# Performance work log

Measured on AMD Instinct MI355X. Metric: run time of the kernel, lower is better.

The kernel has to match this reference:

```python
import jax, jax.numpy as jnp
import numpy as np

V, E, H, D = 50257, 512, 512, 2  # vocab, embed_dim, hidden_dim, depth (nlayers)
B, S, T = 32, 60, 48             # batch, encoder len, target len


def setup_inputs() -> dict:
    key = jax.random.key(0)
    ks = jax.random.split(key, 9)
    return {
        "enc_h": jax.random.normal(ks[0], (B, S, 2 * H), jnp.float32),
        "prev_s": jax.random.normal(ks[1], (B, H), jnp.float32),
        "target": jax.random.randint(ks[2], (T, B), 0, V),
        "embed_W": jax.random.normal(ks[3], (V, E), jnp.float32) * 0.02,
        "attn_W": jax.random.normal(ks[4], (2 * H, H), jnp.float32) * (1.0 / np.sqrt(2 * H)),
        "attn_b": jnp.zeros((H,), jnp.float32),
        "inp_W": jax.random.normal(ks[5], (E, 2 * H), jnp.float32) * (1.0 / np.sqrt(E)),
        "inp_b": jnp.zeros((2 * H,), jnp.float32),
        "cell_W": jax.random.normal(ks[6], (D, H, 2 * H), jnp.float32) * (1.0 / np.sqrt(H)),
        "cell_b": jnp.zeros((D, 2 * H), jnp.float32),
        "out_W": jax.random.normal(ks[7], (H, V), jnp.float32) * (1.0 / np.sqrt(H)),
        "out_b": jnp.zeros((V,), jnp.float32),
    }


def reference(enc_h, prev_s, target, embed_W, attn_W, attn_b,
              inp_W, inp_b, cell_W, cell_b, out_W, out_b):
    # target: T x B -> embeddings T x B x E
    emb = embed_W[target]
    # enc_h is fixed across timesteps: precompute attention keys (B x S x H)
    energy = jnp.tanh(enc_h @ attn_W + attn_b)
    depth = cell_W.shape[0]

    def step(s, x_t):
        # attention: scores B x S, ctx B x 2H
        scores = jnp.einsum("bsh,bh->bs", energy, s)
        alpha = jax.nn.softmax(scores, axis=-1)
        ctx = jnp.einsum("bs,bsd->bd", alpha, enc_h)
        ctx_e = ctx[:, :E]  # module uses ctx[:, 0:embed_dim] (j never updated)
        for l in range(depth):  # small fixed depth loop
            Ws = (s * ctx_e) @ cell_W[l] + cell_b[l]
            if l == 0:
                Ws = Ws + x_t @ inp_W + inp_b
            hh, tt = jnp.split(Ws, 2, axis=1)
            hh = jnp.tanh(hh)
            tt = jax.nn.sigmoid(tt)
            s = hh * tt + s * (1.0 - tt)  # highway gate (dropout p=0)
        return s, s

    _, dec_h = jax.lax.scan(step, prev_s, emb)  # T x B x H
    return dec_h @ out_W + out_b  # T x B x V
```

## Files before the change

kernel.cpp:

```cpp
#include <hip/hip_runtime.h>
#include <hip/hip_bf16.h>
#include <math.h>

#define B_ 32
#define S_ 60
#define T_ 48
#define H_ 512
#define E_ 512
#define V_ 50257
#define NPAD 50432
#define EPI_LD 260
#define NTILE ((NPAD / 256) * 12)

typedef __attribute__((ext_vector_type(8))) short bf16x8v;
typedef __attribute__((ext_vector_type(4))) float f32x4v;
typedef __attribute__((ext_vector_type(4))) float f32x4a __attribute__((aligned(4)));
typedef __attribute__((ext_vector_type(4))) unsigned int u32x4;

__device__ inline unsigned short f2bf(float f) {
    union { float f; unsigned u; } v; v.f = f;
    unsigned r = v.u + 0x7fffu + ((v.u >> 16) & 1u);
    return (unsigned short)(r >> 16);
}
__device__ inline float bflo(unsigned u) { return __uint_as_float(u << 16); }

__device__ inline void gload_lds16(const void* g, void* l) {
    __builtin_amdgcn_global_load_lds(
        (const __attribute__((address_space(1))) unsigned int*)g,
        (__attribute__((address_space(3))) unsigned int*)l, 16, 0, 0);
}

__device__ __forceinline__ float ld_coh_f32_nw(const float* p) {
    float r;
    asm volatile("global_load_dword %0, %1, off sc0 sc1"
                 : "=v"(r) : "v"(p) : "memory");
    return r;
}
__device__ __forceinline__ void st_coh_f32(float* p, float v) {
    asm volatile("global_store_dword %0, %1, off sc0 sc1"
                 :: "v"(p), "v"(v) : "memory");
}
__device__ __forceinline__ void st_coh_u16(unsigned short* p, unsigned int v) {
    asm volatile("global_store_short %0, %1, off sc0 sc1"
                 :: "v"(p), "v"(v) : "memory");
}
__device__ __forceinline__ void st_coh_u32(int* p, int v) {
    asm volatile("global_store_dword %0, %1, off sc0 sc1"
                 :: "v"(p), "v"(v) : "memory");
}
__device__ __forceinline__ void st_coh_u64(unsigned long long* p, unsigned long long v) {
    asm volatile("global_store_dwordx2 %0, %1, off sc0 sc1"
                 :: "v"(p), "v"(v) : "memory");
}
__device__ __forceinline__ int ld_coh_u32(const int* p) {
    int r;
    asm volatile("global_load_dword %0, %1, off sc0 sc1\n\ts_waitcnt vmcnt(0)"
                 : "=v"(r) : "v"(p) : "memory");
    return r;
}
__device__ __forceinline__ u32x4 ld_cohx4(const void* p) {
    u32x4 r;
    asm volatile("global_load_dwordx4 %0, %1, off sc0 sc1"
                 : "=v"(r) : "v"(p) : "memory");
    return r;
}

__device__ __forceinline__ void gbar(int* flags, int idx, int bi) {
    asm volatile("s_waitcnt vmcnt(0)" ::: "memory");
    __syncthreads();
    if (threadIdx.x == 0)
        st_coh_u32(&flags[idx * 32 + bi], 1);
    if (threadIdx.x < 64) {
        const int* fp = &flags[idx * 32 + (threadIdx.x & 31)];
        for (;;) {
            int v = ld_coh_u32(fp);
            if (__all(v != 0)) break;
            __builtin_amdgcn_s_sleep(1);
        }
    }
    __syncthreads();
}

template<int ACT, bool GATHER>
__device__ void gemm_body(const float* __restrict__ A, const float* __restrict__ Bm,
                          const float* __restrict__ bias, float* __restrict__ C,
                          int N, int K, int lda, const int* __restrict__ gidx,
                          int cb, int rb, float (*As)[128], float (*Bs)[128])
{
    const int tid = threadIdx.x;
    const int am = tid >> 1;
    const int ak = (tid & 1) * 4;
    const int arow = rb + am;
    const float* Arow;
    if (GATHER) Arow = A + (size_t)gidx[arow] * lda;
    else        Arow = A + (size_t)arow * lda;

    const int bk = tid >> 5;
    const int bn = (tid & 31) * 4;

    const int tx = tid & 15, ty = tid >> 4;
    float acc[8][8];
    #pragma unroll
    for (int i = 0; i < 8; i++)
        #pragma unroll
        for (int j = 0; j < 8; j++) acc[i][j] = 0.f;

    for (int k0 = 0; k0 < K; k0 += 8) {
        float4 av = *(const float4*)(Arow + k0 + ak);
        float4 bv = *(const float4*)(Bm + (size_t)(k0 + bk) * N + cb + bn);
        __syncthreads();
        As[ak + 0][am] = av.x; As[ak + 1][am] = av.y;
        As[ak + 2][am] = av.z; As[ak + 3][am] = av.w;
        Bs[bk][bn + 0] = bv.x; Bs[bk][bn + 1] = bv.y;
        Bs[bk][bn + 2] = bv.z; Bs[bk][bn + 3] = bv.w;
        __syncthreads();

        #pragma unroll
        for (int k = 0; k < 8; k++) {
            float a[8], b[8];
            *(float4*)(a)     = *(const float4*)&As[k][ty * 4];
            *(float4*)(a + 4) = *(const float4*)&As[k][ty * 4 + 64];
            *(float4*)(b)     = *(const float4*)&Bs[k][tx * 4];
            *(float4*)(b + 4) = *(const float4*)&Bs[k][tx * 4 + 64];
            #pragma unroll
            for (int i = 0; i < 8; i++)
                #pragma unroll
                for (int j = 0; j < 8; j++)
                    acc[i][j] = fmaf(a[i], b[j], acc[i][j]);
        }
    }

    #pragma unroll
    for (int i = 0; i < 8; i++) {
        int row = rb + ((i < 4) ? (ty * 4 + i) : (64 + ty * 4 + (i - 4)));
        #pragma unroll
        for (int j = 0; j < 8; j++) {
            int col = cb + ((j < 4) ? (tx * 4 + j) : (64 + tx * 4 + (j - 4)));
            float v = acc[i][j] + bias[col];
            if (ACT == 1) v = tanhf(v);
            C[(size_t)row * N + col] = v;
        }
    }
}

__global__ __launch_bounds__(256)
void gemm_pro(const float* __restrict__ enc_h, const float* __restrict__ attn_W,
              const float* __restrict__ attn_b, float* __restrict__ energy,
              const float* __restrict__ embed_W, const float* __restrict__ inp_W,
              const float* __restrict__ inp_b, float* __restrict__ pre,
              const int* __restrict__ target, int* __restrict__ cnt)
{
    __shared__ float As[8][128];
    __shared__ float Bs[8][128];
    const int bx = blockIdx.x;
    if (bx < 60) {
        const int cb = (bx & 3) * 128, rb = (bx >> 2) * 128;
        gemm_body<1, false>(enc_h, attn_W, attn_b, energy,
                            512, 1024, 1024, nullptr, cb, rb, As, Bs);
    } else if (bx < 156) {
        const int b2 = bx - 60;
        const int cb = (b2 & 7) * 128, rb = (b2 >> 3) * 128;
        gemm_body<0, true>(embed_W, inp_W, inp_b, pre,
                           1024, 512, 512, target, cb, rb, As, Bs);
    } else {
        for (int i = threadIdx.x; i < 144 * 32; i += 256)
            st_coh_u32(&cnt[i], 0);
    }
}

union __align__(16) ScanSM {
    struct {
        float eL[S_][H_];
        float part[8 * 32 * 36];
        float sCol[512];
    } s;
    float til[2 * 32 * 33];
    char g[49152];
};

template<int LI>
__device__ __forceinline__ void highway(
    int t, int bi, int tid, int lane, int wv,
    const bf16x8v (&wf)[2][2],
    const unsigned short* __restrict__ xsrc,
    unsigned short* __restrict__ xG1,
    const float* __restrict__ ctxG,
    float* __restrict__ sG,
    unsigned short* __restrict__ dec_b,
    const float* __restrict__ pre,
    float cbh, float cbt,
    float* part, float* sCol)
{
    const int l15 = lane & 15, lc = lane >> 4;
    const int b = tid >> 4, hi = tid & 15;
    const int h = bi * 16 + hi;

    float cxv = 0.f, prh = 0.f, prt = 0.f;
    if (LI == 0) {
        cxv = ld_coh_f32_nw(ctxG + (size_t)b * 512 + h);
        const float* pr = pre + ((size_t)t * B_ + b) * 1024;
        prh = pr[h]; prt = pr[h + 512];
    }

    u32x4 xr[2][2][2];
    #pragma unroll
    for (int ktl = 0; ktl < 2; ++ktl)
        #pragma unroll
        for (int pl = 0; pl < 2; ++pl)
            #pragma unroll
            for (int mt = 0; mt < 2; ++mt) {
                int ch = (((wv * 2 + ktl) * 2 + pl) * 4 + lc) * 32 + mt * 16 + l15;
                xr[ktl][pl][mt] = ld_cohx4(xsrc + (size_t)ch * 8);
            }
    asm volatile("s_waitcnt vmcnt(0)" ::: "memory");
    __builtin_amdgcn_sched_barrier(0);

    f32x4v acc[2][2];
    #pragma unroll
    for (int mt = 0; mt < 2; ++mt)
        #pragma unroll
        for (int nt = 0; nt < 2; ++nt) acc[mt][nt] = (f32x4v)0.f;

    #pragma unroll
    for (int ktl = 0; ktl < 2; ++ktl)
        #pragma unroll
        for (int pl = 0; pl < 2; ++pl)
            #pragma unroll
            for (int mt = 0; mt < 2; ++mt) {
                bf16x8v xv = *(bf16x8v*)&xr[ktl][pl][mt];
                #pragma unroll
                for (int nt = 0; nt < 2; ++nt)
                    acc[mt][nt] = __builtin_amdgcn_mfma_f32_16x16x32_bf16(
                        wf[ktl][nt], xv, acc[mt][nt], 0, 0, 0);
            }

    #pragma unroll
    for (int mt = 0; mt < 2; ++mt)
        #pragma unroll
        for (int nt = 0; nt < 2; ++nt)
            *(f32x4v*)&part[(wv * 32 + mt * 16 + l15) * 36 + nt * 16 + lc * 4] = acc[mt][nt];
    __syncthreads();

    float rh = 0.f, rt = 0.f;
    #pragma unroll
    for (int w = 0; w < 8; ++w) {
        rh += part[(w * 32 + b) * 36 + hi];
        rt += part[(w * 32 + b) * 36 + 16 + hi];
    }
    float ph = rh + cbh, pt = rt + cbt;
    if (LI == 0) { ph += prh; pt += prt; }
    float hh = tanhf(ph);
    float tg = 1.f / (1.f + __expf(-pt));
    float sold = sCol[tid];
    float sn = hh * tg + sold * (1.f - tg);
    sCol[tid] = sn;
    if (LI == 0) {
        float x1 = sn * cxv;
        unsigned short xh = f2bf(x1);
        unsigned short xl = f2bf(x1 - bflo((unsigned)xh));
        int kt = h >> 5, lc2 = (h >> 3) & 3, jj = h & 7;
        int ch = (kt * 8 + lc2) * 32 + b;
        st_coh_u16(xG1 + (size_t)ch * 8 + jj, xh);
        st_coh_u16(xG1 + (size_t)(ch + 128) * 8 + jj, xl);
    } else {
        st_coh_f32(sG + ((size_t)bi * 32 + b) * 16 + hi, sn);
        st_coh_u16(dec_b + ((size_t)bi * 1536 + (size_t)t * B_ + b) * 16 + hi,
                   f2bf(sn));
    }
}

__global__ __launch_bounds__(512, 2)
void scan_tr(const float* __restrict__ energy, const float* __restrict__ enc_h,
             const float* __restrict__ prev_s, const float* __restrict__ pre,
             const float* __restrict__ cell_W, const float* __restrict__ cell_b,
             unsigned short* __restrict__ dec_b,
             const float* __restrict__ outW, unsigned short* __restrict__ Wt,
             float* __restrict__ ctxG, float* __restrict__ sG,
             unsigned short* __restrict__ xG0, unsigned short* __restrict__ xG1,
             int* __restrict__ cnt,
             const float* __restrict__ out_b, float* __restrict__ out)
{
    __shared__ ScanSM sm;
    const int tid = threadIdx.x;

    if (blockIdx.x >= B_) {
        const int hb = blockIdx.x - B_;
        const int g = tid >> 8;
        const int tt0 = tid & 255;
        const int r = tt0 >> 3, c4 = (tt0 & 7) * 4;
        float* til = sm.til;
        #pragma unroll 1
        for (int j = 0; j < 57; ++j) {
            const int tt = hb * 2 + g + j * 448;
            const bool act = tt < (NPAD / 32) * 16;
            int n0 = 0, k0 = 0;
            if (act) {
                n0 = (tt >> 4) * 32;
                k0 = (tt & 15) * 32;
                #pragma unroll
                for (int jj = 0; jj < 4; ++jj) {
                    int n = n0 + c4 + jj;
                    til[(g * 32 + r) * 33 + c4 + jj] =
                        (n < V_) ? __builtin_nontemporal_load(&outW[(size_t)(k0 + r) * V_ + n]) : 0.f;
                }
            }
            __syncthreads();
            if (act) {
                const int n = n0 + r;
                unsigned lo = (unsigned)f2bf(til[(g * 32 + c4 + 0) * 33 + r])
                            | ((unsigned)f2bf(til[(g * 32 + c4 + 1) * 33 + r]) << 16);
                unsigned hi2 = (unsigned)f2bf(til[(g * 32 + c4 + 2) * 33 + r])
                             | ((unsigned)f2bf(til[(g * 32 + c4 + 3) * 33 + r]) << 16);
                unsigned long long ov = (unsigned long long)lo | ((unsigned long long)hi2 << 32);
                st_coh_u64((unsigned long long*)&Wt[(size_t)n * 512 + k0 + c4], ov);
            }
            __syncthreads();
        }

        {
            int* hF = cnt + 101 * 32;
            asm volatile("s_waitcnt vmcnt(0)" ::: "memory");
            __syncthreads();
            if (tid == 0) st_coh_u32(&hF[hb], 1);
            if (tid < 64) {
                for (;;) {
                    int ok = 1;
                    #pragma unroll
                    for (int q = 0; q < 4; ++q) {
                        int idx = (tid & 63) + q * 64;
                        int v = (idx < 224) ? ld_coh_u32(&hF[idx]) : 1;
                        ok &= (v != 0);
                    }
                    if (__all(ok)) break;
                    __builtin_amdgcn_s_sleep(16);
                }
            }
            __syncthreads();
        }

        {
            short* As_wt  = (short*)sm.g;
            short* Bs_dec = (short*)(sm.g + 32768);
            float* epi    = (float*)sm.g;
            const int lane = tid & 63, w = tid >> 6;
            const int wm = w >> 2, wn = w & 3;
            int* sF = cnt + 100 * 32;

#define STAGE_TILE(bix, kt, rb, cb) do {                                      \
            short* Ab_ = As_wt + (bix) * 8192;                                \
            short* Bb_ = Bs_dec + (bix) * 4096;                               \
            _Pragma("unroll")                                                 \
            for (int j_ = 0; j_ < 2; ++j_) {                                  \
                int rg_ = w * 2 + j_;                                         \
                int row_ = rg_ * 16 + (lane >> 2);                            \
                int kc_ = (lane & 3) ^ (row_ & 3);                            \
                gload_lds16(Wt + ((size_t)((cb) + row_) * 512 + (kt) * 32 + kc_ * 8), \
                            Ab_ + rg_ * 512);                                 \
            }                                                                 \
            {                                                                 \
                int row_ = w * 16 + (lane >> 2);                              \
                int kc_ = (lane & 3) ^ (row_ & 3);                            \
                gload_lds16(dec_b + (((size_t)((kt) * 2 + (kc_ >> 1)) * 1536 + ((rb) + row_)) * 16 \
                                     + (kc_ & 1) * 8),                        \
                            Bb_ + w * 512);                                   \
            }                                                                 \
        } while (0)

            #pragma unroll 1
            for (int i = hb; i < NTILE; i += 224) {
                const int rbi = i / 197;
                const int rb  = rbi * 128;
                const int cb  = (i % 197) * 256;
                const int need = rbi * 4 + 4;

                if (tid < 64) {
                    const int* fp = &sF[tid & 31];
                    for (;;) {
                        int v = ld_coh_u32(fp);
                        if (__all(v >= need)) break;
                        __builtin_amdgcn_s_sleep(32);
                    }
                }
                __syncthreads();

                f32x4v acc[4][4];
                #pragma unroll
                for (int mi = 0; mi < 4; ++mi)
                    #pragma unroll
                    for (int ni = 0; ni < 4; ++ni) acc[mi][ni] = (f32x4v)0.f;

                STAGE_TILE(0, 0, rb, cb);

                #pragma unroll 1
                for (int it = 0; it < 16; ++it) {
                    const int cur = it & 1;
                    __builtin_amdgcn_s_barrier();
                    asm volatile("" ::: "memory");
                    if (it < 15) {
                        STAGE_TILE(cur ^ 1, it + 1, rb, cb);
                        asm volatile("s_waitcnt vmcnt(3)" ::: "memory");
                    } else {
                        asm volatile("s_waitcnt vmcnt(0)" ::: "memory");
                    }
                    __builtin_amdgcn_s_barrier();
                    asm volatile("" ::: "memory");

                    const short* Ab = As_wt + cur * 8192;
                    const short* Bb = Bs_dec + cur * 4096;
                    bf16x8v af[4], bf[4];
                    const int lc = lane >> 4;
                    #pragma unroll
                    for (int ni = 0; ni < 4; ++ni) {
                        int r_ = wn * 64 + ni * 16 + (lane & 15);
                        af[ni] = *(const bf16x8v*)&Ab[r_ * 32 + ((lc ^ (r_ & 3)) * 8)];
                    }
                    #pragma unroll
                    for (int mi = 0; mi < 4; ++mi) {
                        int r_ = wm * 64 + mi * 16 + (lane & 15);
                        bf[mi] = *(const bf16x8v*)&Bb[r_ * 32 + ((lc ^ (r_ & 3)) * 8)];
                    }
                    #pragma unroll
                    for (int mi = 0; mi < 4; ++mi)
                        #pragma unroll
                        for (int ni = 0; ni < 4; ++ni)
                            acc[mi][ni] = __builtin_amdgcn_mfma_f32_16x16x32_bf16(
                                af[ni], bf[mi], acc[mi][ni], 0, 0, 0);
                }

                const int c4e = (tid & 63) * 4;
                const bool fullcols = (cb + 256 <= V_);
                f32x4v bq = (f32x4v)0.f;
                if (fullcols) {
                    float4 t4 = *(const float4*)(out_b + cb + c4e);
                    bq[0] = t4.x; bq[1] = t4.y; bq[2] = t4.z; bq[3] = t4.w;
                }
                #pragma unroll
                for (int mi = 0; mi < 4; ++mi) {
                    __syncthreads();
                    #pragma unroll
                    for (int ni = 0; ni < 4; ++ni) {
                        const int er = wm * 16 + (lane & 15);
                        const int ec = wn * 64 + ni * 16 + (lane >> 4) * 4;
                        *(f32x4v*)&epi[er * EPI_LD + ec] = acc[mi][ni];
                    }
                    __syncthreads();
                    #pragma unroll
                    for (int j = 0; j < 4; ++j) {
                        const int rr = w + j * 8;
                        const int orow = rb + (rr >> 4) * 64 + mi * 16 + (rr & 15);
                        f32x4v v = *(const f32x4v*)&epi[rr * EPI_LD + c4e];
                        if (fullcols) {
                            v += bq;
                            *(f32x4a*)(out + (size_t)orow * V_ + cb + c4e) = v;
                        } else {
                            #pragma unroll
                            for (int vv = 0; vv < 4; ++vv) {
                                const int col = cb + c4e + vv;
                                if (col < V_)
                                    out[(size_t)orow * V_ + col] = v[vv] + out_b[col];
                            }
                        }
                    }
                }
            }
#undef STAGE_TILE
        }
        return;
    }

    const int bi = blockIdx.x;
    const int lane = tid & 63, wv = tid >> 6;
    float (*eL)[H_] = sm.s.eL;
    float* part   = sm.s.part;
    float* sA     = part;
    float* scoreL = part + 512;
    float* alphaL = part + 576;
    float* sCol   = sm.s.sCol;
    int*   sF     = cnt + 100 * 32;

    for (int i = tid; i < S_ * H_ / 4; i += 512) {
        int s = i >> 7, h4 = (i & 127) * 4;
        *(float4*)&eL[s][h4] = *(const float4*)&energy[((size_t)bi * S_ + s) * 512 + h4];
    }

    bf16x8v wf0[2][2], wf1[2][2];
    {
        const int l15 = lane & 15, lc = lane >> 4;
        #pragma unroll
        for (int ktl = 0; ktl < 2; ++ktl)
            #pragma unroll
            for (int nt = 0; nt < 2; ++nt) {
                const int kb = (wv * 2 + ktl) * 32 + lc * 8;
                const int n  = nt * 512 + bi * 16 + l15;
                #pragma unroll
                for (int jj = 0; jj < 8; ++jj) {
                    wf0[ktl][nt][jj] = (short)f2bf(cell_W[((size_t)(kb + jj)) * 1024 + n]);
                    wf1[ktl][nt][jj] = (short)f2bf(cell_W[((size_t)(512 + kb + jj)) * 1024 + n]);
                }
            }
    }
    const int hME = bi * 16 + (tid & 15);
    sCol[tid] = prev_s[(size_t)(tid >> 4) * 512 + hME];
    const float cb0h = cell_b[hME],        cb0t = cell_b[512 + hME];
    const float cb1h = cell_b[1024 + hME], cb1t = cell_b[1536 + hME];

    #pragma unroll 1
    for (int t = 0; t < T_; ++t) {
        float sAv;
        if (t == 0) {
            sAv = prev_s[(size_t)bi * 512 + tid];
            __syncthreads();
            sA[tid] = sAv;
            __syncthreads();
        } else {
            const int* fp = &sF[tid >> 4];
            for (;;) {
                int v = ld_coh_u32(fp);
                if (v >= t) break;
                __builtin_amdgcn_s_sleep(1);
            }
            sAv = ld_coh_f32_nw(sG + ((size_t)(tid >> 4) * 32 + bi) * 16 + (tid & 15));
            __syncthreads();
            asm volatile("s_waitcnt vmcnt(0)" ::: "memory");
            sA[tid] = sAv;
            __syncthreads();
        }

        #pragma unroll 1
        for (int sp = 0; sp < 4; ++sp) {
            const int s0 = wv + sp * 16;
            const int s1 = s0 + 8;
            const bool has1 = (sp < 3) | (wv < 4);
            const float* e0 = &eL[s0][lane];
            const float* e1 = &eL[has1 ? s1 : s0][lane];
            float a0 = 0.f, a1 = 0.f;
            #pragma unroll
            for (int j = 0; j < 8; ++j) {
                float sv = sA[lane + j * 64];
                a0 = fmaf(e0[j * 64], sv, a0);
                a1 = fmaf(e1[j * 64], sv, a1);
            }
            #pragma unroll
            for (int off = 32; off; off >>= 1) {
                a0 += __shfl_xor(a0, off, 64);
                a1 += __shfl_xor(a1, off, 64);
            }
            if (lane == 0) {
                scoreL[s0] = a0;
                if (has1) scoreL[s1] = a1;
            }
        }
        __syncthreads();
        if (wv == 0) {
            float v = (lane < S_) ? scoreL[lane] : -3.4e38f;
            float m = v;
            #pragma unroll
            for (int off = 32; off; off >>= 1) m = fmaxf(m, __shfl_xor(m, off, 64));
            float e = (lane < S_) ? __expf(v - m) : 0.f;
            float su = e;
            #pragma unroll
            for (int off = 32; off; off >>= 1) su += __shfl_xor(su, off, 64);
            if (lane < S_) alphaL[lane] = e / su;
        }
        __syncthreads();
        {
            float a = 0.f;
            const float* ep = enc_h + (size_t)bi * S_ * 1024 + tid;
            #pragma unroll 20
            for (int s = 0; s < S_; ++s) a = fmaf(alphaL[s], ep[(size_t)s * 1024], a);
            st_coh_f32(ctxG + (size_t)bi * 512 + tid, a);
            float x0 = a * sA[tid];
            unsigned short xh = f2bf(x0);
            unsigned short xl = f2bf(x0 - bflo((unsigned)xh));
            int kt = tid >> 5, lc2 = (tid >> 3) & 3, jj = tid & 7;
            int ch = (kt * 8 + lc2) * 32 + bi;
            st_coh_u16(xG0 + (size_t)ch * 8 + jj, xh);
            st_coh_u16(xG0 + (size_t)(ch + 128) * 8 + jj, xl);
        }
        gbar(cnt, 2 * t + 0, bi);
        highway<0>(t, bi, tid, lane, wv, wf0, xG0, xG1, ctxG, sG, dec_b, pre,
                   cb0h, cb0t, part, sCol);
        gbar(cnt, 2 * t + 1, bi);
        highway<1>(t, bi, tid, lane, wv, wf1, xG1, xG1, ctxG, sG, dec_b, pre,
                   cb1h, cb1t, part, sCol);
        asm volatile("s_waitcnt vmcnt(0)" ::: "memory");
        __syncthreads();
        if (tid == 0)
            st_coh_u32(&sF[bi], t + 1);
    }
}

extern "C" void kernel_launch(void* const* d_in, const int* in_sizes, int n_in,
                              void* d_out, int out_size, void* d_ws, size_t ws_size,
                              hipStream_t stream)
{
    const float* enc_h   = (const float*)d_in[0];
    const float* prev_s  = (const float*)d_in[1];
    const int*   target  = (const int*)  d_in[2];
    const float* embed_W = (const float*)d_in[3];
    const float* attn_W  = (const float*)d_in[4];
    const float* attn_b  = (const float*)d_in[5];
    const float* inp_W   = (const float*)d_in[6];
    const float* inp_b   = (const float*)d_in[7];
    const float* cell_W  = (const float*)d_in[8];
    const float* cell_b  = (const float*)d_in[9];
    const float* out_W   = (const float*)d_in[10];
    const float* out_b   = (const float*)d_in[11];
    float* out = (float*)d_out;

    float* ws = (float*)d_ws;
    float* energy = ws;
    float* pre    = energy + (size_t)B_ * S_ * H_;
    float* ctxG   = pre + (size_t)T_ * B_ * 2 * H_;
    float* sG     = ctxG + (size_t)B_ * H_;
    int*   cnt    = (int*)(sG + (size_t)B_ * H_);
    unsigned short* dec_b = (unsigned short*)(cnt + 144 * 32);
    unsigned short* xG0   = dec_b + (size_t)T_ * B_ * H_;
    unsigned short* xG1   = xG0 + (size_t)2 * B_ * H_;
    unsigned short* Wt    = xG1 + (size_t)2 * B_ * H_;

    gemm_pro<<<157, 256, 0, stream>>>(enc_h, attn_W, attn_b, energy,
                                      embed_W, inp_W, inp_b, pre, target, cnt);

    scan_tr<<<256, 512, 0, stream>>>(energy, enc_h, prev_s, pre, cell_W, cell_b,
                                     dec_b, out_W, Wt, ctxG, sG, xG0, xG1, cnt,
                                     out_b, out);
}
```

Before: 855.8 us.

## Split energy GEMM into 64-row tiles and aggregate scan progress flag

The prologue energy GEMM now uses 64-row tiles, doubling its block count so more CUs work on it. Output-projection blocks now poll a single aggregated progress counter, written by batch block 0 once all sF flags reach a step and again after the scan ends, instead of each lane polling 32 per-batch flags. This is meant to shorten the prologue critical path and cut polling traffic during the scan, but the aggregate counter adds a serial dependency on block 0 and may lag true progress.

```diff
diff --git a/kernel.cpp b/kernel.cpp
--- a/kernel.cpp
+++ b/kernel.cpp
@@ -81,15 +81,16 @@
     __syncthreads();
 }
 
-template<int ACT, bool GATHER>
+template<int ACT, bool GATHER, int MR>
 __device__ void gemm_body(const float* __restrict__ A, const float* __restrict__ Bm,
                           const float* __restrict__ bias, float* __restrict__ C,
                           int N, int K, int lda, const int* __restrict__ gidx,
                           int cb, int rb, float (*As)[128], float (*Bs)[128])
 {
     const int tid = threadIdx.x;
-    const int am = tid >> 1;
+    const int am = (MR == 128) ? (tid >> 1) : ((tid & 127) >> 1);
     const int ak = (tid & 1) * 4;
+    const bool aact = (MR == 128) || (tid < 128);
     const int arow = rb + am;
     const float* Arow;
     if (GATHER) Arow = A + (size_t)gidx[arow] * lda;
@@ -99,31 +100,38 @@
     const int bn = (tid & 31) * 4;
 
     const int tx = tid & 15, ty = tid >> 4;
-    float acc[8][8];
+    float acc[MR / 16][8];
     #pragma unroll
-    for (int i = 0; i < 8; i++)
+    for (int i = 0; i < MR / 16; i++)
         #pragma unroll
         for (int j = 0; j < 8; j++) acc[i][j] = 0.f;
 
     for (int k0 = 0; k0 < K; k0 += 8) {
-        float4 av = *(const float4*)(Arow + k0 + ak);
-        float4 bv = *(const float4*)(Bm + (size_t)(k0 + bk) * N + cb + bn);
+        float4 av, bv;
+        if (aact) av = *(const float4*)(Arow + k0 + ak);
+        bv = *(const float4*)(Bm + (size_t)(k0 + bk) * N + cb + bn);
         __syncthreads();
-        As[ak + 0][am] = av.x; As[ak + 1][am] = av.y;
-        As[ak + 2][am] = av.z; As[ak + 3][am] = av.w;
+        if (aact) {
+            As[ak + 0][am] = av.x; As[ak + 1][am] = av.y;
+            As[ak + 2][am] = av.z; As[ak + 3][am] = av.w;
+        }
         Bs[bk][bn + 0] = bv.x; Bs[bk][bn + 1] = bv.y;
         Bs[bk][bn + 2] = bv.z; Bs[bk][bn + 3] = bv.w;
         __syncthreads();
 
         #pragma unroll
         for (int k = 0; k < 8; k++) {
-            float a[8], b[8];
-            *(float4*)(a)     = *(const float4*)&As[k][ty * 4];
-            *(float4*)(a + 4) = *(const float4*)&As[k][ty * 4 + 64];
+            float a[MR / 16], b[8];
+            if constexpr (MR == 128) {
+                *(float4*)(a)     = *(const float4*)&As[k][ty * 4];
+                *(float4*)(a + 4) = *(const float4*)&As[k][ty * 4 + 64];
+            } else {
+                *(float4*)(a)     = *(const float4*)&As[k][ty * 4];
+            }
             *(float4*)(b)     = *(const float4*)&Bs[k][tx * 4];
             *(float4*)(b + 4) = *(const float4*)&Bs[k][tx * 4 + 64];
             #pragma unroll
-            for (int i = 0; i < 8; i++)
+            for (int i = 0; i < MR / 16; i++)
                 #pragma unroll
                 for (int j = 0; j < 8; j++)
                     acc[i][j] = fmaf(a[i], b[j], acc[i][j]);
@@ -131,8 +139,12 @@
     }
 
     #pragma unroll
-    for (int i = 0; i < 8; i++) {
-        int row = rb + ((i < 4) ? (ty * 4 + i) : (64 + ty * 4 + (i - 4)));
+    for (int i = 0; i < MR / 16; i++) {
+        int row;
+        if constexpr (MR == 128)
+            row = rb + ((i < 4) ? (ty * 4 + i) : (64 + ty * 4 + (i - 4)));
+        else
+            row = rb + ty * 4 + i;
         #pragma unroll
         for (int j = 0; j < 8; j++) {
             int col = cb + ((j < 4) ? (tx * 4 + j) : (64 + tx * 4 + (j - 4)));
@@ -153,15 +165,15 @@
     __shared__ float As[8][128];
     __shared__ float Bs[8][128];
     const int bx = blockIdx.x;
-    if (bx < 60) {
-        const int cb = (bx & 3) * 128, rb = (bx >> 2) * 128;
-        gemm_body<1, false>(enc_h, attn_W, attn_b, energy,
-                            512, 1024, 1024, nullptr, cb, rb, As, Bs);
-    } else if (bx < 156) {
-        const int b2 = bx - 60;
+    if (bx < 120) {
+        const int cb = (bx & 3) * 128, rb = (bx >> 2) * 64;
+        gemm_body<1, false, 64>(enc_h, attn_W, attn_b, energy,
+                                512, 1024, 1024, nullptr, cb, rb, As, Bs);
+    } else if (bx < 216) {
+        const int b2 = bx - 120;
         const int cb = (b2 & 7) * 128, rb = (b2 >> 3) * 128;
-        gemm_body<0, true>(embed_W, inp_W, inp_b, pre,
-                           1024, 512, 512, target, cb, rb, As, Bs);
+        gemm_body<0, true, 128>(embed_W, inp_W, inp_b, pre,
+                                1024, 512, 512, target, cb, rb, As, Bs);
     } else {
         for (int i = threadIdx.x; i < 144 * 32; i += 256)
             st_coh_u32(&cnt[i], 0);
@@ -282,6 +294,7 @@
 {
     __shared__ ScanSM sm;
     const int tid = threadIdx.x;
+    int* aggF = cnt + 108 * 32;
 
     if (blockIdx.x >= B_) {
         const int hb = blockIdx.x - B_;
@@ -344,7 +357,6 @@
             float* epi    = (float*)sm.g;
             const int lane = tid & 63, w = tid >> 6;
             const int wm = w >> 2, wn = w & 3;
-            int* sF = cnt + 100 * 32;
 
 #define STAGE_TILE(bix, kt, rb, cb) do {                                      \
             short* Ab_ = As_wt + (bix) * 8192;                                \
@@ -374,11 +386,10 @@
                 const int need = rbi * 4 + 4;
 
                 if (tid < 64) {
-                    const int* fp = &sF[tid & 31];
                     for (;;) {
-                        int v = ld_coh_u32(fp);
+                        int v = ld_coh_u32(aggF);
                         if (__all(v >= need)) break;
-                        __builtin_amdgcn_s_sleep(32);
+                        __builtin_amdgcn_s_sleep(16);
                     }
                 }
                 __syncthreads();
@@ -524,6 +535,8 @@
             asm volatile("s_waitcnt vmcnt(0)" ::: "memory");
             sA[tid] = sAv;
             __syncthreads();
+            if (bi == 0 && tid == 0)
+                st_coh_u32(aggF, t);
         }
 
         #pragma unroll 1
@@ -587,6 +600,20 @@
         __syncthreads();
         if (tid == 0)
             st_coh_u32(&sF[bi], t + 1);
+    }
+
+    if (bi == 0) {
+        if (tid < 64) {
+            const int* fp2 = &sF[tid & 31];
+            for (;;) {
+                int v = ld_coh_u32(fp2);
+                if (__all(v >= T_)) break;
+                __builtin_amdgcn_s_sleep(1);
+            }
+        }
+        __syncthreads();
+        if (tid == 0)
+            st_coh_u32(aggF, T_);
     }
 }
 
@@ -619,7 +646,7 @@
     unsigned short* xG1   = xG0 + (size_t)2 * B_ * H_;
     unsigned short* Wt    = xG1 + (size_t)2 * B_ * H_;
 
-    gemm_pro<<<157, 256, 0, stream>>>(enc_h, attn_W, attn_b, energy,
+    gemm_pro<<<217, 256, 0, stream>>>(enc_h, attn_W, attn_b, energy,
                                       embed_W, inp_W, inp_b, pre, target, cnt);
 
     scan_tr<<<256, 512, 0, stream>>>(energy, enc_h, prev_s, pre, cell_W, cell_b,
```

Result: faster. 789.8 us (-7.7%).
